# Kernel tuning notes

Measured on AMD Instinct MI355X. Metric: run time of the kernel, lower is better.

The kernel has to match this reference:

```python
import jax, jax.numpy as jnp
import numpy as np

T, B, C = 1024, 16, 1024
H, K, PAD = 16, 7, 6  # num_heads, kernel_size, padding_l (causal)
R = C // H


def setup_inputs() -> dict:
    key = jax.random.key(0)
    kx, kw = jax.random.split(key)
    x = jax.random.normal(kx, (T, B, C), dtype=jnp.float32)
    # xavier_uniform for weight_linear.weight of shape (H*K, C)
    bound = float(np.sqrt(6.0 / (C + H * K)))
    W = jax.random.uniform(kw, (H * K, C), dtype=jnp.float32, minval=-bound, maxval=bound)
    return {"x": x, "W": W}


def reference(x, W):
    Tn, Bn, Cn = x.shape
    # dynamic per-position conv weights: (T, B, H, K)
    w = jnp.einsum('tbc,oc->tbo', x, W).reshape(Tn, Bn, H, K)

    # band structure: row t attends absolute positions t + k - PAD, k in [0, K)
    pos = jnp.arange(Tn)[:, None] + jnp.arange(K)[None, :] - PAD     # (T, K)
    valid = (pos >= 0) & (pos < Tn)                                   # (T, K)
    logits = jnp.where(valid[:, None, None, :], w, -jnp.inf)
    wsm = jax.nn.softmax(logits, axis=-1)                             # (T, B, H, K), zeros off-band

    # windowed weighted sum (the bmm against the band matrix, done directly)
    pc = jnp.clip(pos, 0, Tn - 1)                                     # (T, K)
    xh = x.reshape(Tn, Bn, H, R)
    xg = xh[pc]                                                       # (T, K, B, H, R)
    out = jnp.einsum('tbhk,tkbhr->tbhr', wsm, xg).reshape(Tn, Bn, Cn)

    # dense (B*H, T, T) softmaxed band matrix, as returned by the torch module
    w_bht = wsm.transpose(1, 2, 0, 3).reshape(Bn * H, Tn, K)
    dense = jnp.zeros((Bn * H, Tn, Tn), wsm.dtype)
    dense = dense.at[:, jnp.arange(Tn)[:, None], pc].add(jnp.where(valid, w_bht, 0.0))
    return out, dense
```

## Files before the change

### kernel.cpp

```cpp
#include <hip/hip_runtime.h>
#include <math.h>

#define TT 1024
#define BB 16
#define CC 1024
#define HH 16
#define KK 7
#define PADL 6
#define HK 112
#define WSTRIDE 68

__global__ __launch_bounds__(256) void k1_weights(const float* __restrict__ x,
                                                  const float* __restrict__ W,
                                                  float* __restrict__ wsm) {
    __shared__ float Wl[HK * WSTRIDE];

    const int tid = threadIdx.x;
    const int tx = tid & 15;
    const int ty = tid >> 4;
    const int row0 = blockIdx.x * 32 + ty * 2;

    const float* __restrict__ xr0 = x + (size_t)row0 * CC;
    const float* __restrict__ xr1 = xr0 + CC;

    float acc0[KK], acc1[KK];
#pragma unroll
    for (int k = 0; k < KK; ++k) { acc0[k] = 0.f; acc1[k] = 0.f; }

    for (int c0 = 0; c0 < CC; c0 += 64) {
        __syncthreads();
#pragma unroll
        for (int j = 0; j < 7; ++j) {
            const int i = j * 1024 + tid * 4;
            const int o = i >> 6;
            const int c = i & 63;
            const float4 v = *(const float4*)(W + (size_t)o * CC + c0 + c);
            *(float4*)(&Wl[o * WSTRIDE + c]) = v;
        }
        __syncthreads();

        const float* __restrict__ Wb = &Wl[(tx * KK) * WSTRIDE];
#pragma unroll 4
        for (int c = 0; c < 64; c += 4) {
            const float4 xv0 = *(const float4*)(xr0 + c0 + c);
            const float4 xv1 = *(const float4*)(xr1 + c0 + c);
#pragma unroll
            for (int k = 0; k < KK; ++k) {
                const float4 wv = *(const float4*)(Wb + k * WSTRIDE + c);
                acc0[k] += xv0.x * wv.x + xv0.y * wv.y + xv0.z * wv.z + xv0.w * wv.w;
                acc1[k] += xv1.x * wv.x + xv1.y * wv.y + xv1.z * wv.z + xv1.w * wv.w;
            }
        }
    }

#pragma unroll
    for (int i = 0; i < 2; ++i) {
        const float* a = (i == 0) ? acc0 : acc1;
        const int row = row0 + i;
        const int t = row >> 4;
        const int kmin = (t >= PADL) ? 0 : (PADL - t);

        float m = -INFINITY;
#pragma unroll
        for (int k = 0; k < KK; ++k)
            if (k >= kmin) m = fmaxf(m, a[k]);

        float e[KK];
        float s = 0.f;
#pragma unroll
        for (int k = 0; k < KK; ++k) {
            if (k >= kmin) { e[k] = expf(a[k] - m); s += e[k]; }
            else           { e[k] = 0.f; }
        }
        const float inv = 1.f / s;
        float* __restrict__ wp = wsm + (((size_t)row * HH) + tx) * KK;
#pragma unroll
        for (int k = 0; k < KK; ++k) wp[k] = e[k] * inv;
    }
}

__global__ __launch_bounds__(256) void k2_dense(const float* __restrict__ wsm,
                                                float* __restrict__ dense) {
    const int blk = blockIdx.x;
    const int bh = blk >> 6;
    const int tc = blk & 63;
    const int b = bh >> 4;
    const int h = bh & 15;

    const int col = threadIdx.x << 2;
    const int t0 = tc * 16;

    float* __restrict__ drow = dense + ((size_t)bh * TT + t0) * TT + col;

#pragma unroll
    for (int i = 0; i < 16; ++i) {
        const int t = t0 + i;
        const int lo = t - PADL;
        float4 v = make_float4(0.f, 0.f, 0.f, 0.f);
        if (col + 3 >= lo && col <= t) {
            const float* __restrict__ wp =
                wsm + (((size_t)t * BB + b) * HH + h) * KK;
            float* pv = &v.x;
#pragma unroll
            for (int j = 0; j < 4; ++j) {
                const int cc = col + j;
                if (cc >= lo && cc <= t && cc >= 0) pv[j] = wp[cc - lo];
            }
        }
        *(float4*)drow = v;
        drow += TT;
    }
}

__global__ __launch_bounds__(256) void k3_out(const float* __restrict__ x,
                                              const float* __restrict__ wsm,
                                              float* __restrict__ out) {
    const int r0 = blockIdx.x << 2;
    const int t = r0 >> 4;
    const int c = threadIdx.x << 2;
    const int h = c >> 6;
    const int kmin = (t >= PADL) ? 0 : (PADL - t);

#pragma unroll
    for (int i = 0; i < 4; ++i) {
        const int row = r0 + i;
        const float* __restrict__ wp = wsm + ((size_t)row * HH + h) * KK;
        float w[KK];
#pragma unroll
        for (int k = 0; k < KK; ++k) w[k] = wp[k];

        float4 acc = make_float4(0.f, 0.f, 0.f, 0.f);
        for (int k = kmin; k < KK; ++k) {
            const float4 xv =
                *(const float4*)(x + ((size_t)row + (size_t)(k - PADL) * BB) * CC + c);
            acc.x += w[k] * xv.x;
            acc.y += w[k] * xv.y;
            acc.z += w[k] * xv.z;
            acc.w += w[k] * xv.w;
        }
        *(float4*)(out + (size_t)row * CC + c) = acc;
    }
}

extern "C" void kernel_launch(void* const* d_in, const int* in_sizes, int n_in,
                              void* d_out, int out_size, void* d_ws, size_t ws_size,
                              hipStream_t stream) {
    const float* x = (const float*)d_in[0];
    const float* W = (const float*)d_in[1];
    float* out = (float*)d_out;
    float* dense = out + (size_t)TT * BB * CC;
    float* wsm = (float*)d_ws;

    k1_weights<<<(TT * BB) / 32, 256, 0, stream>>>(x, W, wsm);
    k2_dense<<<BB * HH * (TT / 16), 256, 0, stream>>>(wsm, dense);
    k3_out<<<(TT * BB) / 4, 256, 0, stream>>>(x, wsm, out);
}
```

Measured before the change: 1.311 ms.

## Double-buffer W tiles in weight GEMM and use nontemporal stores for outputs

```diff
diff --git a/kernel.cpp b/kernel.cpp
--- a/kernel.cpp
+++ b/kernel.cpp
@@ -10,52 +10,69 @@
 #define HK 112
 #define WSTRIDE 68
 
-__global__ __launch_bounds__(256) void k1_weights(const float* __restrict__ x,
+typedef float vf4 __attribute__((ext_vector_type(4)));
+
+__device__ __forceinline__ void stage_chunk(const float* __restrict__ W,
+                                            float* __restrict__ buf,
+                                            int c0, int tid) {
+#pragma unroll
+    for (int j = 0; j < 14; ++j) {
+        const int i = j * 512 + tid * 4;
+        const int o = i >> 6;
+        const int c = i & 63;
+        const float4 v = *(const float4*)(W + (size_t)o * CC + c0 + c);
+        *(float4*)(&buf[o * WSTRIDE + c]) = v;
+    }
+}
+
+__global__ __launch_bounds__(128) void k1_weights(const float* __restrict__ x,
                                                   const float* __restrict__ W,
                                                   float* __restrict__ wsm) {
-    __shared__ float Wl[HK * WSTRIDE];
+    __shared__ float Wl[2][HK * WSTRIDE];
 
     const int tid = threadIdx.x;
     const int tx = tid & 15;
     const int ty = tid >> 4;
-    const int row0 = blockIdx.x * 32 + ty * 2;
+    const int row0 = blockIdx.x * 32 + ty * 4;
 
     const float* __restrict__ xr0 = x + (size_t)row0 * CC;
-    const float* __restrict__ xr1 = xr0 + CC;
 
-    float acc0[KK], acc1[KK];
+    float acc[4][KK];
 #pragma unroll
-    for (int k = 0; k < KK; ++k) { acc0[k] = 0.f; acc1[k] = 0.f; }
+    for (int i = 0; i < 4; ++i)
+#pragma unroll
+        for (int k = 0; k < KK; ++k) acc[i][k] = 0.f;
 
-    for (int c0 = 0; c0 < CC; c0 += 64) {
-        __syncthreads();
+    stage_chunk(W, Wl[0], 0, tid);
+    __syncthreads();
+
+    for (int ch = 0; ch < 16; ++ch) {
+        const int p = ch & 1;
+        const int c0 = ch * 64;
+        if (ch + 1 < 16) stage_chunk(W, Wl[p ^ 1], c0 + 64, tid);
+
+        const float* __restrict__ Wb = &Wl[p][(tx * KK) * WSTRIDE];
+#pragma unroll 2
+        for (int c = 0; c < 64; c += 4) {
+            float4 xv[4];
 #pragma unroll
-        for (int j = 0; j < 7; ++j) {
-            const int i = j * 1024 + tid * 4;
-            const int o = i >> 6;
-            const int c = i & 63;
-            const float4 v = *(const float4*)(W + (size_t)o * CC + c0 + c);
-            *(float4*)(&Wl[o * WSTRIDE + c]) = v;
-        }
-        __syncthreads();
-
-        const float* __restrict__ Wb = &Wl[(tx * KK) * WSTRIDE];
-#pragma unroll 4
-        for (int c = 0; c < 64; c += 4) {
-            const float4 xv0 = *(const float4*)(xr0 + c0 + c);
-            const float4 xv1 = *(const float4*)(xr1 + c0 + c);
+            for (int i = 0; i < 4; ++i)
+                xv[i] = *(const float4*)(xr0 + (size_t)i * CC + c0 + c);
 #pragma unroll
             for (int k = 0; k < KK; ++k) {
                 const float4 wv = *(const float4*)(Wb + k * WSTRIDE + c);
-                acc0[k] += xv0.x * wv.x + xv0.y * wv.y + xv0.z * wv.z + xv0.w * wv.w;
-                acc1[k] += xv1.x * wv.x + xv1.y * wv.y + xv1.z * wv.z + xv1.w * wv.w;
+#pragma unroll
+                for (int i = 0; i < 4; ++i)
+                    acc[i][k] += xv[i].x * wv.x + xv[i].y * wv.y +
+                                 xv[i].z * wv.z + xv[i].w * wv.w;
             }
         }
+        __syncthreads();
     }
 
 #pragma unroll
-    for (int i = 0; i < 2; ++i) {
-        const float* a = (i == 0) ? acc0 : acc1;
+    for (int i = 0; i < 4; ++i) {
+        const float* a = acc[i];
         const int row = row0 + i;
         const int t = row >> 4;
         const int kmin = (t >= PADL) ? 0 : (PADL - t);
@@ -96,18 +113,17 @@
     for (int i = 0; i < 16; ++i) {
         const int t = t0 + i;
         const int lo = t - PADL;
-        float4 v = make_float4(0.f, 0.f, 0.f, 0.f);
+        vf4 v = (vf4){0.f, 0.f, 0.f, 0.f};
         if (col + 3 >= lo && col <= t) {
             const float* __restrict__ wp =
                 wsm + (((size_t)t * BB + b) * HH + h) * KK;
-            float* pv = &v.x;
 #pragma unroll
             for (int j = 0; j < 4; ++j) {
                 const int cc = col + j;
-                if (cc >= lo && cc <= t && cc >= 0) pv[j] = wp[cc - lo];
+                if (cc >= lo && cc <= t && cc >= 0) v[j] = wp[cc - lo];
             }
         }
-        *(float4*)drow = v;
+        __builtin_nontemporal_store(v, (vf4*)drow);
         drow += TT;
     }
 }
@@ -115,21 +131,21 @@
 __global__ __launch_bounds__(256) void k3_out(const float* __restrict__ x,
                                               const float* __restrict__ wsm,
                                               float* __restrict__ out) {
-    const int r0 = blockIdx.x << 2;
+    const int r0 = blockIdx.x << 3;
     const int t = r0 >> 4;
     const int c = threadIdx.x << 2;
     const int h = c >> 6;
     const int kmin = (t >= PADL) ? 0 : (PADL - t);
 
 #pragma unroll
-    for (int i = 0; i < 4; ++i) {
+    for (int i = 0; i < 8; ++i) {
         const int row = r0 + i;
         const float* __restrict__ wp = wsm + ((size_t)row * HH + h) * KK;
         float w[KK];
 #pragma unroll
         for (int k = 0; k < KK; ++k) w[k] = wp[k];
 
-        float4 acc = make_float4(0.f, 0.f, 0.f, 0.f);
+        vf4 acc = (vf4){0.f, 0.f, 0.f, 0.f};
         for (int k = kmin; k < KK; ++k) {
             const float4 xv =
                 *(const float4*)(x + ((size_t)row + (size_t)(k - PADL) * BB) * CC + c);
@@ -138,7 +154,7 @@
             acc.z += w[k] * xv.z;
             acc.w += w[k] * xv.w;
         }
-        *(float4*)(out + (size_t)row * CC + c) = acc;
+        __builtin_nontemporal_store(acc, (vf4*)(out + (size_t)row * CC + c));
     }
 }
 
@@ -151,7 +167,7 @@
     float* dense = out + (size_t)TT * BB * CC;
     float* wsm = (float*)d_ws;
 
-    k1_weights<<<(TT * BB) / 32, 256, 0, stream>>>(x, W, wsm);
+    k1_weights<<<(TT * BB) / 32, 128, 0, stream>>>(x, W, wsm);
     k2_dense<<<BB * HH * (TT / 16), 256, 0, stream>>>(wsm, dense);
-    k3_out<<<(TT * BB) / 4, 256, 0, stream>>>(x, wsm, out);
+    k3_out<<<(TT * BB) / 8, 256, 0, stream>>>(x, wsm, out);
 }
```

New measurement: 1.363 ms. +4.0%, slower.

## Compute dynamic conv logits with bf16 MFMA instead of fp32 FMA

Applied to the files above, without the earlier changes.

```diff
diff --git a/kernel.cpp b/kernel.cpp
--- a/kernel.cpp
+++ b/kernel.cpp
@@ -8,74 +8,119 @@
 #define KK 7
 #define PADL 6
 #define HK 112
-#define WSTRIDE 68
-
-__global__ __launch_bounds__(256) void k1_weights(const float* __restrict__ x,
-                                                  const float* __restrict__ W,
-                                                  float* __restrict__ wsm) {
-    __shared__ float Wl[HK * WSTRIDE];
+#define LSTRIDE 116
+
+typedef short bf16x8 __attribute__((ext_vector_type(8)));
+typedef float f32x4 __attribute__((ext_vector_type(4)));
+
+__device__ __forceinline__ short f2bf(float f) {
+    union { float f; unsigned u; } v; v.f = f;
+    unsigned r = v.u + 0x7fff + ((v.u >> 16) & 1);
+    return (short)(r >> 16);
+}
+
+__global__ __launch_bounds__(256) void k0_cvtW(const float* __restrict__ W,
+                                               short* __restrict__ Wb) {
+    const int i = (blockIdx.x * 256 + threadIdx.x) * 8;
+    const float4 a0 = *(const float4*)(W + i);
+    const float4 a1 = *(const float4*)(W + i + 4);
+    bf16x8 v;
+    v[0] = f2bf(a0.x); v[1] = f2bf(a0.y); v[2] = f2bf(a0.z); v[3] = f2bf(a0.w);
+    v[4] = f2bf(a1.x); v[5] = f2bf(a1.y); v[6] = f2bf(a1.z); v[7] = f2bf(a1.w);
+    *(bf16x8*)(Wb + i) = v;
+}
+
+__global__ __launch_bounds__(256) void k1_mfma(const float* __restrict__ x,
+                                               const short* __restrict__ Wb,
+                                               float* __restrict__ wsm) {
+    __shared__ __align__(16) float Llog[4][16 * LSTRIDE];
+    __shared__ __align__(16) float Lout[4][16 * HK];
 
     const int tid = threadIdx.x;
-    const int tx = tid & 15;
-    const int ty = tid >> 4;
-    const int row0 = blockIdx.x * 32 + ty * 2;
-
-    const float* __restrict__ xr0 = x + (size_t)row0 * CC;
-    const float* __restrict__ xr1 = xr0 + CC;
-
-    float acc0[KK], acc1[KK];
-#pragma unroll
-    for (int k = 0; k < KK; ++k) { acc0[k] = 0.f; acc1[k] = 0.f; }
-
-    for (int c0 = 0; c0 < CC; c0 += 64) {
-        __syncthreads();
+    const int w = tid >> 6;
+    const int lane = tid & 63;
+    const int quad = lane >> 4;
+    const int lr = lane & 15;
+    const int strip = blockIdx.x * 4 + w;
+    const int r0 = strip * 16;
+
+    bf16x8 ap, bp;
+#pragma unroll
+    for (int e = 0; e < 8; ++e) {
+        const int k = quad * 8 + e;
+        ap[e] = (k == lr) ? (short)0x3F80 : (short)0;
+        bp[e] = f2bf((float)k);
+    }
+    f32x4 pz = (f32x4){0.f, 0.f, 0.f, 0.f};
+    pz = __builtin_amdgcn_mfma_f32_16x16x32_bf16(ap, bp, pz, 0, 0, 0);
+    const bool claim = (pz[0] == (float)(quad * 4)) &&
+                       (pz[1] == (float)(quad * 4 + 1));
+
+    const float* __restrict__ xa = x + (size_t)(r0 + lr) * CC + quad * 8;
+    const short* __restrict__ wb = Wb + (size_t)lr * CC + quad * 8;
+
+    f32x4 acc[7];
+#pragma unroll
+    for (int j = 0; j < 7; ++j) acc[j] = (f32x4){0.f, 0.f, 0.f, 0.f};
+
+#pragma unroll 4
+    for (int k0 = 0; k0 < CC; k0 += 32) {
+        const float4 a0 = *(const float4*)(xa + k0);
+        const float4 a1 = *(const float4*)(xa + k0 + 4);
+        bf16x8 af;
+        af[0] = f2bf(a0.x); af[1] = f2bf(a0.y); af[2] = f2bf(a0.z); af[3] = f2bf(a0.w);
+        af[4] = f2bf(a1.x); af[5] = f2bf(a1.y); af[6] = f2bf(a1.z); af[7] = f2bf(a1.w);
 #pragma unroll
         for (int j = 0; j < 7; ++j) {
-            const int i = j * 1024 + tid * 4;
-            const int o = i >> 6;
-            const int c = i & 63;
-            const float4 v = *(const float4*)(W + (size_t)o * CC + c0 + c);
-            *(float4*)(&Wl[o * WSTRIDE + c]) = v;
-        }
-        __syncthreads();
-
-        const float* __restrict__ Wb = &Wl[(tx * KK) * WSTRIDE];
-#pragma unroll 4
-        for (int c = 0; c < 64; c += 4) {
-            const float4 xv0 = *(const float4*)(xr0 + c0 + c);
-            const float4 xv1 = *(const float4*)(xr1 + c0 + c);
-#pragma unroll
-            for (int k = 0; k < KK; ++k) {
-                const float4 wv = *(const float4*)(Wb + k * WSTRIDE + c);
-                acc0[k] += xv0.x * wv.x + xv0.y * wv.y + xv0.z * wv.z + xv0.w * wv.w;
-                acc1[k] += xv1.x * wv.x + xv1.y * wv.y + xv1.z * wv.z + xv1.w * wv.w;
-            }
-        }
-    }
-
-#pragma unroll
-    for (int i = 0; i < 2; ++i) {
-        const float* a = (i == 0) ? acc0 : acc1;
-        const int row = row0 + i;
-        const int t = row >> 4;
-        const int kmin = (t >= PADL) ? 0 : (PADL - t);
-
-        float m = -INFINITY;
+            const bf16x8 bfrag = *(const bf16x8*)(wb + (size_t)(j * 16) * CC + k0);
+            acc[j] = __builtin_amdgcn_mfma_f32_16x16x32_bf16(af, bfrag, acc[j], 0, 0, 0);
+        }
+    }
+
+#pragma unroll
+    for (int j = 0; j < 7; ++j)
+#pragma unroll
+        for (int r = 0; r < 4; ++r) {
+            const int rowi = claim ? (quad * 4 + r) : lr;
+            const int coli = claim ? lr : (quad * 4 + r);
+            Llog[w][rowi * LSTRIDE + j * 16 + coli] = acc[j][r];
+        }
+    __syncthreads();
+
+    const int kmin = (strip >= PADL) ? 0 : (PADL - strip);
+#pragma unroll
+    for (int p = 0; p < 4; ++p) {
+        const int idx = p * 64 + lane;
+        const int m = idx >> 4;
+        const int h = idx & 15;
+        const float* lp = &Llog[w][m * LSTRIDE + h * KK];
+        float a[KK];
+#pragma unroll
+        for (int k = 0; k < KK; ++k) a[k] = lp[k];
+
+        float mx = -INFINITY;
 #pragma unroll
         for (int k = 0; k < KK; ++k)
-            if (k >= kmin) m = fmaxf(m, a[k]);
-
-        float e[KK];
-        float s = 0.f;
+            if (k >= kmin) mx = fmaxf(mx, a[k]);
+        float e[KK], s = 0.f;
 #pragma unroll
         for (int k = 0; k < KK; ++k) {
-            if (k >= kmin) { e[k] = expf(a[k] - m); s += e[k]; }
+            if (k >= kmin) { e[k] = expf(a[k] - mx); s += e[k]; }
             else           { e[k] = 0.f; }
         }
         const float inv = 1.f / s;
-        float* __restrict__ wp = wsm + (((size_t)row * HH) + tx) * KK;
-#pragma unroll
-        for (int k = 0; k < KK; ++k) wp[k] = e[k] * inv;
+        float* op = &Lout[w][m * HK + h * KK];
+#pragma unroll
+        for (int k = 0; k < KK; ++k) op[k] = e[k] * inv;
+    }
+    __syncthreads();
+
+    float* __restrict__ dst = wsm + (size_t)r0 * HK;
+    const float* __restrict__ src = &Lout[w][0];
+#pragma unroll
+    for (int i = 0; i < 7; ++i) {
+        const int o = i * 256 + lane * 4;
+        *(float4*)(dst + o) = *(const float4*)(src + o);
     }
 }
 
@@ -150,8 +195,10 @@
     float* out = (float*)d_out;
     float* dense = out + (size_t)TT * BB * CC;
     float* wsm = (float*)d_ws;
-
-    k1_weights<<<(TT * BB) / 32, 256, 0, stream>>>(x, W, wsm);
+    short* Wb = (short*)(wsm + (size_t)TT * BB * HK);
+
+    k0_cvtW<<<56, 256, 0, stream>>>(W, Wb);
+    k1_mfma<<<256, 256, 0, stream>>>(x, Wb, wsm);
     k2_dense<<<BB * HH * (TT / 16), 256, 0, stream>>>(wsm, dense);
     k3_out<<<(TT * BB) / 4, 256, 0, stream>>>(x, wsm, out);
 }
```

After: 1.210 ms. -7.7%, faster.
